# Optimization experiments

Measured on AMD Instinct MI355X. Metric: run time of the kernel, lower is better.

## Reference

```python
import jax, jax.numpy as jnp
import numpy as np

HID = 1024     # hidden_dim
HEADS = 8      # num_heads
HD = HID // HEADS  # head_dim = 128
MD = 8         # manifold_dim
L = 3          # num_layers
B, S = 8, 1024
EPS = 1e-7
BALL_MAX = 1.0 - 1e-5  # clamp inside Poincare ball (|curvature| = 1)


def expmap0(v):
    """Hyperbolic exponential map at origin, curvature -1 (Poincare ball)."""
    n = jnp.sqrt(jnp.sum(v * v, axis=-1, keepdims=True))
    n = jnp.maximum(n, EPS)
    return jnp.tanh(n) * v / n


def logmap0(y):
    """Hyperbolic logarithm map at origin, curvature -1 (Poincare ball)."""
    n = jnp.sqrt(jnp.sum(y * y, axis=-1, keepdims=True))
    n_c = jnp.clip(n, EPS, BALL_MAX)
    return jnp.arctanh(n_c) * y / n_c


def setup_inputs() -> dict:
    key = jax.random.key(0)
    ks = jax.random.split(key, 6)
    sc = 0.02
    return {
        "x": jax.random.normal(ks[0], (B, S, HID), dtype=jnp.float32),
        "W_qkv": jax.random.normal(ks[1], (HID, 3 * HID), dtype=jnp.float32) * sc,
        "b_qkv": jnp.zeros((3 * HID,), dtype=jnp.float32),
        "W_pinv": jax.random.normal(ks[2], (HID, MD), dtype=jnp.float32) * sc,
        "b_pinv": jnp.zeros((MD,), dtype=jnp.float32),
        "W_attn": jax.random.normal(ks[3], (L, MD, HID), dtype=jnp.float32) * sc,
        "b_attn": jnp.zeros((L, HID), dtype=jnp.float32),
        "W_out": jax.random.normal(ks[4], (HID, HID), dtype=jnp.float32) * sc,
        "b_out": jnp.zeros((HID,), dtype=jnp.float32),
    }


def reference(x, W_qkv, b_qkv, W_pinv, b_pinv, W_attn, b_attn, W_out, b_out):
    inv_sqrt_d = 1.0 / np.sqrt(HD).astype(np.float32)
    cur = x
    for l in range(L):
        qkv = jnp.einsum('bsh,hd->bsd', cur, W_qkv) + b_qkv  # [B,S,3*HID]
        q, k, v = jnp.split(qkv, 3, axis=-1)
        # [B,S,HID] -> [B,HEADS,S,HD]
        def heads(t):
            return t.reshape(B, S, HEADS, HD).transpose(0, 2, 1, 3)
        q, k, v = heads(q), heads(k), heads(v)
        # geometric 'flow': hyperbolic retraction of Q/K onto the Poincare ball
        # (parallel transport at the origin is identity)
        qf = expmap0(q)
        kf = expmap0(k)
        scores = jnp.einsum('bhqd,bhkd->bhqk', qf, kf) * inv_sqrt_d
        att = jax.nn.softmax(scores, axis=-1)
        o = jnp.einsum('bhqk,bhkd->bhqd', att, v)  # [B,H,S,HD]
        o = o.transpose(0, 2, 1, 3).reshape(B, S, HID)
        # project to manifold coords, then per-layer pattern projection back
        m = jnp.einsum('bsh,hm->bsm', o, W_pinv) + b_pinv           # [B,S,MD]
        upd = jnp.einsum('bsm,mh->bsh', m, W_attn[l]) + b_attn[l]   # [B,S,HID]
        cur = cur + upd
    return jnp.einsum('bsh,hd->bsd', cur, W_out) + b_out
```

## Files before the change

### kernel.cpp

```cpp
#include <hip/hip_runtime.h>
#include <hip/hip_bf16.h>
#include <hip/hip_fp8.h>
#include <cstdint>

typedef __hip_bfloat16 bf16;
typedef __bf16 b8 __attribute__((ext_vector_type(8)));
typedef float f4v __attribute__((ext_vector_type(4)));
typedef short s8v __attribute__((ext_vector_type(8)));
typedef int i8v __attribute__((ext_vector_type(8)));

#define DEVI static __device__ __forceinline__

DEVI void gload16(const void* g, void* l) {
  __builtin_amdgcn_global_load_lds(
      (const __attribute__((address_space(1))) void*)(uintptr_t)g,
      (__attribute__((address_space(3))) void*)(uint32_t)(uintptr_t)l,
      16, 0, 0);
}

DEVI f4v mfma_bf16(b8 a, b8 b, f4v c) {
  return __builtin_amdgcn_mfma_f32_16x16x32_bf16(a, b, c, 0, 0, 0);
}

DEVI f4v mfma_fp8(i8v a, i8v b, f4v c) {
  return __builtin_amdgcn_mfma_scale_f32_16x16x128_f8f6f4(
      a, b, c, 0, 0, 0, 0x7F7F7F7F, 0, 0x7F7F7F7F);
}

DEVI uint8_t to_fp8(float f) {
  __hip_fp8_e4m3 v(f);
  return v.__x;
}

__global__ void prep_kernel(const float* __restrict__ x, float* __restrict__ cur,
                            bf16* __restrict__ curb, uint8_t* __restrict__ curf8) {
  int i = (blockIdx.x * 256 + threadIdx.x) * 4;
  float4 v = *(const float4*)(x + i);
  *(float4*)(cur + i) = v;
  __hip_bfloat162 a, b;
  a.x = __float2bfloat16(v.x); a.y = __float2bfloat16(v.y);
  b.x = __float2bfloat16(v.z); b.y = __float2bfloat16(v.w);
  *(__hip_bfloat162*)(curb + i) = a;
  *(__hip_bfloat162*)(curb + i + 2) = b;
  uint32_t p = (uint32_t)to_fp8(v.x) | ((uint32_t)to_fp8(v.y) << 8) |
               ((uint32_t)to_fp8(v.z) << 16) | ((uint32_t)to_fp8(v.w) << 24);
  *(uint32_t*)(curf8 + i) = p;
}

__global__ void transpose_cast(const float* __restrict__ in, bf16* __restrict__ out,
                               int R, int C) {
  __shared__ float tile[32][33];
  int c0 = blockIdx.x * 32, r0 = blockIdx.y * 32;
  int tx = threadIdx.x & 31, ty = threadIdx.x >> 5;
  for (int rr = ty; rr < 32; rr += 8)
    tile[rr][tx] = in[(size_t)(r0 + rr) * C + c0 + tx];
  __syncthreads();
  for (int cc = ty; cc < 32; cc += 8)
    out[(size_t)(c0 + cc) * R + r0 + tx] = __float2bfloat16(tile[tx][cc]);
}

__global__ void transpose_cast_fp8(const float* __restrict__ in,
                                   uint8_t* __restrict__ out, int R, int C) {
  __shared__ float tile[32][33];
  int c0 = blockIdx.x * 32, r0 = blockIdx.y * 32;
  int tx = threadIdx.x & 31, ty = threadIdx.x >> 5;
  for (int rr = ty; rr < 32; rr += 8)
    tile[rr][tx] = in[(size_t)(r0 + rr) * C + c0 + tx];
  __syncthreads();
  for (int cc = ty; cc < 32; cc += 8)
    out[(size_t)(c0 + cc) * R + r0 + tx] = to_fp8(tile[tx][cc]);
}

__global__ __launch_bounds__(256, 3)
void gemm_qkv_fp8(const uint8_t* __restrict__ A, const uint8_t* __restrict__ Bt,
                  const float* __restrict__ bias, bf16* __restrict__ Qo,
                  bf16* __restrict__ Ko, bf16* __restrict__ Vto, int M, int N,
                  int K) {
  __shared__ uint8_t As[128 * 128];
  __shared__ uint8_t Bs[128 * 128];
  __shared__ float red[2][128];
  const int t = threadIdx.x;
  const int w = t >> 6, lane = t & 63;
  const int lm = lane & 15, qd = lane >> 4;
  const int m0 = blockIdx.x * 128, n0 = blockIdx.y * 128;
  const int wm = (w & 1) * 64, wn = (w >> 1) * 64;

  const uint8_t* Ag = A + (size_t)m0 * K;
  const uint8_t* Bg = Bt + (size_t)n0 * K;

  f4v acc[4][4];
  f4v zero = {0.f, 0.f, 0.f, 0.f};
#pragma unroll
  for (int i = 0; i < 4; i++)
#pragma unroll
    for (int j = 0; j < 4; j++) acc[i][j] = zero;

  for (int k0 = 0; k0 < K; k0 += 128) {
#pragma unroll
    for (int c = 0; c < 4; c++) {
      int s = c * 256 + t;
      int r = s >> 3;
      int kc = (s & 7) ^ (r & 7);
      gload16(Ag + (size_t)r * K + k0 + kc * 16, &As[s * 16]);
      gload16(Bg + (size_t)r * K + k0 + kc * 16, &Bs[s * 16]);
    }
    __syncthreads();
    i8v af[4], bfr[4];
#pragma unroll
    for (int tm = 0; tm < 4; tm++) {
      int row = wm + tm * 16 + lm;
      int ch = (qd * 2) ^ (row & 7);
      union { int4 q[2]; i8v v; } u;
      u.q[0] = *(const int4*)&As[row * 128 + ch * 16];
      u.q[1] = *(const int4*)&As[row * 128 + (ch ^ 1) * 16];
      af[tm] = u.v;
    }
#pragma unroll
    for (int tn = 0; tn < 4; tn++) {
      int row = wn + tn * 16 + lm;
      int ch = (qd * 2) ^ (row & 7);
      union { int4 q[2]; i8v v; } u;
      u.q[0] = *(const int4*)&Bs[row * 128 + ch * 16];
      u.q[1] = *(const int4*)&Bs[row * 128 + (ch ^ 1) * 16];
      bfr[tn] = u.v;
    }
#pragma unroll
    for (int tm = 0; tm < 4; tm++)
#pragma unroll
      for (int tn = 0; tn < 4; tn++)
        acc[tm][tn] = mfma_fp8(af[tm], bfr[tn], acc[tm][tn]);
    __syncthreads();
  }

  const int part = n0 >> 10;
  const int hh = (n0 >> 7) & 7;
  if (part == 2) {
#pragma unroll
    for (int tm = 0; tm < 4; tm++)
#pragma unroll
      for (int tn = 0; tn < 4; tn++) {
        int d = wn + tn * 16 + lm;
        float bv = bias[n0 + d];
        int row0 = m0 + wm + tm * 16 + qd * 4;
        int b = row0 >> 10, s0 = row0 & 1023;
        bf16 vt[4];
#pragma unroll
        for (int r = 0; r < 4; r++) vt[r] = __float2bfloat16(acc[tm][tn][r] + bv);
        *(ushort4*)&Vto[((size_t)(b * 8 + hh)) * 131072 + (size_t)d * 1024 + s0] =
            *(ushort4*)vt;
      }
  } else {
    float bvs[4];
#pragma unroll
    for (int tn = 0; tn < 4; tn++) bvs[tn] = bias[n0 + wn + tn * 16 + lm];
    float ss[4][4];
#pragma unroll
    for (int tm = 0; tm < 4; tm++)
#pragma unroll
      for (int r = 0; r < 4; r++) {
        float s = 0.f;
#pragma unroll
        for (int tn = 0; tn < 4; tn++) {
          float v = acc[tm][tn][r] + bvs[tn];
          s += v * v;
        }
#pragma unroll
        for (int off = 1; off < 16; off <<= 1) s += __shfl_xor(s, off, 64);
        ss[tm][r] = s;
      }
    if (lm == 0) {
#pragma unroll
      for (int tm = 0; tm < 4; tm++)
#pragma unroll
        for (int r = 0; r < 4; r++)
          red[w >> 1][wm + tm * 16 + qd * 4 + r] = ss[tm][r];
    }
    __syncthreads();
    const float qsc = (part == 0) ? 0.08838834764831845f : 1.0f;
    float scr[4][4];
#pragma unroll
    for (int tm = 0; tm < 4; tm++)
#pragma unroll
      for (int r = 0; r < 4; r++) {
        int row = wm + tm * 16 + qd * 4 + r;
        float tot = red[0][row] + red[1][row];
        float nrm = fmaxf(sqrtf(tot), 1e-7f);
        scr[tm][r] = tanhf(nrm) / nrm * qsc;
      }
    bf16* dst = (part == 0) ? Qo : Ko;
#pragma unroll
    for (int tm = 0; tm < 4; tm++)
#pragma unroll
      for (int tn = 0; tn < 4; tn++) {
        int d = wn + tn * 16 + lm;
        int row0 = m0 + wm + tm * 16 + qd * 4;
        int b = row0 >> 10, s0 = row0 & 1023;
#pragma unroll
        for (int r = 0; r < 4; r++)
          dst[(((size_t)(b * 8 + hh)) * 1024 + s0 + r) * 128 + d] =
              __float2bfloat16((acc[tm][tn][r] + bvs[tn]) * scr[tm][r]);
      }
  }
}

__global__ __launch_bounds__(256, 3)
void gemm_bt(const bf16* __restrict__ A, const bf16* __restrict__ Bt,
             const float* __restrict__ bias, float* __restrict__ Cf, int M, int N,
             int K) {
  __shared__ bf16 As[128 * 64];
  __shared__ bf16 Bs[128 * 64];
  const int t = threadIdx.x;
  const int w = t >> 6, lane = t & 63;
  const int lm = lane & 15, qd = lane >> 4;
  const int m0 = blockIdx.x * 128, n0 = blockIdx.y * 128;
  const int wm = (w & 1) * 64, wn = (w >> 1) * 64;

  const bf16* Ag = A + (size_t)m0 * K;
  const bf16* Bg = Bt + (size_t)n0 * K;

  f4v acc[4][4];
  f4v zero = {0.f, 0.f, 0.f, 0.f};
#pragma unroll
  for (int i = 0; i < 4; i++)
#pragma unroll
    for (int j = 0; j < 4; j++) acc[i][j] = zero;

  for (int k0 = 0; k0 < K; k0 += 64) {
#pragma unroll
    for (int c = 0; c < 4; c++) {
      int s = c * 256 + t;
      int r = s >> 3;
      int kc = (s & 7) ^ (r & 7);
      gload16(Ag + (size_t)r * K + k0 + kc * 8, &As[s * 8]);
      gload16(Bg + (size_t)r * K + k0 + kc * 8, &Bs[s * 8]);
    }
    __syncthreads();
#pragma unroll
    for (int ks = 0; ks < 2; ks++) {
      b8 af[4], bfr[4];
#pragma unroll
      for (int tm = 0; tm < 4; tm++) {
        int row = wm + tm * 16 + lm;
        int ch = (ks * 4 + qd) ^ (row & 7);
        af[tm] = *(const b8*)&As[row * 64 + ch * 8];
      }
#pragma unroll
      for (int tn = 0; tn < 4; tn++) {
        int row = wn + tn * 16 + lm;
        int ch = (ks * 4 + qd) ^ (row & 7);
        bfr[tn] = *(const b8*)&Bs[row * 64 + ch * 8];
      }
#pragma unroll
      for (int tm = 0; tm < 4; tm++)
#pragma unroll
        for (int tn = 0; tn < 4; tn++)
          acc[tm][tn] = mfma_bf16(af[tm], bfr[tn], acc[tm][tn]);
    }
    __syncthreads();
  }

#pragma unroll
  for (int tm = 0; tm < 4; tm++)
#pragma unroll
    for (int tn = 0; tn < 4; tn++) {
      int col = n0 + wn + tn * 16 + lm;
      float bv = bias[col];
#pragma unroll
      for (int r = 0; r < 4; r++) {
        int row = m0 + wm + tm * 16 + qd * 4 + r;
        Cf[(size_t)row * N + col] = acc[tm][tn][r] + bv;
      }
    }
}

__global__ __launch_bounds__(256, 2)
void attn_kernel(const bf16* __restrict__ Qf, const bf16* __restrict__ Kf,
                 const bf16* __restrict__ Vt, bf16* __restrict__ O) {
  __shared__ bf16 smem[40960];
  bf16* Ps = smem + 32768;
  const int t = threadIdx.x, w = t >> 6, lane = t & 63;
  const int lm = lane & 15, qd = lane >> 4;
  const int bh = blockIdx.x, qt = blockIdx.y;
  const bf16* Qg = Qf + ((size_t)bh * 1024 + qt * 128) * 128;
  const bf16* Kg = Kf + (size_t)bh * 131072;
  const bf16* Vg = Vt + (size_t)bh * 131072;
  bf16* Pw = Ps + w * 2048;

  auto stage = [&](int kt, int b) {
    bf16* Ksb = smem + b * 16384;
    bf16* Vsb = Ksb + 8192;
#pragma unroll
    for (int c = 0; c < 4; c++) {
      int s = c * 256 + t;
      int r = s >> 4;
      int kc = (s & 15) ^ (r & 7);
      gload16(Kg + (size_t)(kt * 64 + r) * 128 + kc * 8, &Ksb[s * 8]);
      int rv = s >> 3;
      int kv = (s & 7) ^ (rv & 7);
      gload16(Vg + (size_t)rv * 1024 + kt * 64 + kv * 8, &Vsb[s * 8]);
    }
  };

  b8 qfr[2][4];
#pragma unroll
  for (int mt = 0; mt < 2; mt++)
#pragma unroll
    for (int ks = 0; ks < 4; ks++)
      qfr[mt][ks] =
          *(const b8*)(Qg + (size_t)(w * 32 + mt * 16 + lm) * 128 + ks * 32 + qd * 8);

  f4v o[2][8];
  f4v lacc[2];
  f4v zero = {0.f, 0.f, 0.f, 0.f};
#pragma unroll
  for (int mt = 0; mt < 2; mt++) {
    lacc[mt] = zero;
#pragma unroll
    for (int i = 0; i < 8; i++) o[mt][i] = zero;
  }
  union { s8v s; b8 b; } uo;
#pragma unroll
  for (int i = 0; i < 8; i++) uo.s[i] = 0x3F80;
  const b8 ones = uo.b;

  stage(0, 0);
  for (int kt = 0; kt < 16; kt++) {
    const int cb = kt & 1;
    if (kt < 15) {
      stage(kt + 1, cb ^ 1);
      asm volatile("s_waitcnt vmcnt(8)" ::: "memory");
    } else {
      asm volatile("s_waitcnt vmcnt(0)" ::: "memory");
    }
    __builtin_amdgcn_sched_barrier(0);
    __builtin_amdgcn_s_barrier();
    __builtin_amdgcn_sched_barrier(0);
    const bf16* Ks = smem + cb * 16384;
    const bf16* Vs = Ks + 8192;

    f4v sc[2][4];
#pragma unroll
    for (int mt = 0; mt < 2; mt++)
#pragma unroll
      for (int tn = 0; tn < 4; tn++) sc[mt][tn] = zero;
#pragma unroll
    for (int tn = 0; tn < 4; tn++) {
      int krow = tn * 16 + lm;
#pragma unroll
      for (int ks = 0; ks < 4; ks++) {
        int ch = (ks * 4 + qd) ^ (krow & 7);
        b8 kfr = *(const b8*)&Ks[krow * 128 + ch * 8];
        sc[0][tn] = mfma_bf16(qfr[0][ks], kfr, sc[0][tn]);
        sc[1][tn] = mfma_bf16(qfr[1][ks], kfr, sc[1][tn]);
      }
    }
#pragma unroll
    for (int mt = 0; mt < 2; mt++)
#pragma unroll
      for (int tn = 0; tn < 4; tn++)
#pragma unroll
        for (int r = 0; r < 4; r++) {
          int qi = mt * 16 + qd * 4 + r;
          int ch = (tn * 2 + (lm >> 3)) ^ ((qi >> 1) & 7);
          Pw[qi * 64 + ch * 8 + (lm & 7)] = __float2bfloat16(__expf(sc[mt][tn][r]));
        }

    b8 pa[2][2];
#pragma unroll
    for (int mt = 0; mt < 2; mt++)
#pragma unroll
      for (int kv2 = 0; kv2 < 2; kv2++) {
        int qi = mt * 16 + lm;
        int ch = (kv2 * 4 + qd) ^ ((lm >> 1) & 7);
        pa[mt][kv2] = *(const b8*)&Pw[qi * 64 + ch * 8];
      }
#pragma unroll
    for (int mt = 0; mt < 2; mt++)
#pragma unroll
      for (int kv2 = 0; kv2 < 2; kv2++)
        lacc[mt] = mfma_bf16(pa[mt][kv2], ones, lacc[mt]);
#pragma unroll
    for (int tnd = 0; tnd < 8; tnd++) {
      int drow = tnd * 16 + lm;
#pragma unroll
      for (int kv2 = 0; kv2 < 2; kv2++) {
        int ch = (kv2 * 4 + qd) ^ (drow & 7);
        b8 vfr = *(const b8*)&Vs[drow * 64 + ch * 8];
#pragma unroll
        for (int mt = 0; mt < 2; mt++)
          o[mt][tnd] = mfma_bf16(pa[mt][kv2], vfr, o[mt][tnd]);
      }
    }
    __builtin_amdgcn_sched_barrier(0);
    __builtin_amdgcn_s_barrier();
  }

  const int b = bh >> 3, h = bh & 7;
#pragma unroll
  for (int mt = 0; mt < 2; mt++) {
    float rinv[4];
#pragma unroll
    for (int r = 0; r < 4; r++) rinv[r] = 1.0f / lacc[mt][r];
#pragma unroll
    for (int tnd = 0; tnd < 8; tnd++) {
      int d = tnd * 16 + lm;
#pragma unroll
      for (int r = 0; r < 4; r++) {
        int sIdx = qt * 128 + w * 32 + mt * 16 + qd * 4 + r;
        O[((size_t)b * 1024 + sIdx) * 1024 + h * 128 + d] =
            __float2bfloat16(o[mt][tnd][r] * rinv[r]);
      }
    }
  }
}

__global__ __launch_bounds__(256)
void update_kernel(const bf16* __restrict__ O, const float* __restrict__ Wpinv,
                   const float* __restrict__ bpinv, const float* __restrict__ Wattn,
                   const float* __restrict__ battn, float* __restrict__ cur,
                   bf16* __restrict__ curb, uint8_t* __restrict__ curf8) {
  const int row = blockIdx.x;
  const int t = threadIdx.x, w = t >> 6, lane = t & 63;
  const int h0 = t * 4;
  const bf16* orow = O + (size_t)row * 1024;

  bf16 ob[4];
  *(ushort4*)ob = *(const ushort4*)(orow + h0);
  float ov[4];
#pragma unroll
  for (int i = 0; i < 4; i++) ov[i] = __bfloat162float(ob[i]);

  float acc[8];
#pragma unroll
  for (int j = 0; j < 8; j++) acc[j] = 0.f;
#pragma unroll
  for (int i = 0; i < 4; i++) {
    float4 wa = *(const float4*)(Wpinv + (size_t)(h0 + i) * 8);
    float4 wb = *(const float4*)(Wpinv + (size_t)(h0 + i) * 8 + 4);
    acc[0] += ov[i] * wa.x; acc[1] += ov[i] * wa.y;
    acc[2] += ov[i] * wa.z; acc[3] += ov[i] * wa.w;
    acc[4] += ov[i] * wb.x; acc[5] += ov[i] * wb.y;
    acc[6] += ov[i] * wb.z; acc[7] += ov[i] * wb.w;
  }
#pragma unroll
  for (int j = 0; j < 8; j++)
#pragma unroll
    for (int off = 32; off; off >>= 1) acc[j] += __shfl_xor(acc[j], off, 64);
  __shared__ float sm[4][8];
  if (lane == 0) {
#pragma unroll
    for (int j = 0; j < 8; j++) sm[w][j] = acc[j];
  }
  __syncthreads();
  float mv[8];
#pragma unroll
  for (int j = 0; j < 8; j++)
    mv[j] = sm[0][j] + sm[1][j] + sm[2][j] + sm[3][j] + bpinv[j];

  float u[4];
#pragma unroll
  for (int i = 0; i < 4; i++) u[i] = battn[h0 + i];
#pragma unroll
  for (int j = 0; j < 8; j++) {
    float4 wv = *(const float4*)(Wattn + (size_t)j * 1024 + h0);
    u[0] += mv[j] * wv.x; u[1] += mv[j] * wv.y;
    u[2] += mv[j] * wv.z; u[3] += mv[j] * wv.w;
  }
  float4 c4 = *(float4*)(cur + (size_t)row * 1024 + h0);
  c4.x += u[0]; c4.y += u[1]; c4.z += u[2]; c4.w += u[3];
  *(float4*)(cur + (size_t)row * 1024 + h0) = c4;
  bf16 cb[4];
  cb[0] = __float2bfloat16(c4.x); cb[1] = __float2bfloat16(c4.y);
  cb[2] = __float2bfloat16(c4.z); cb[3] = __float2bfloat16(c4.w);
  *(ushort4*)(curb + (size_t)row * 1024 + h0) = *(ushort4*)cb;
  uint32_t p = (uint32_t)to_fp8(c4.x) | ((uint32_t)to_fp8(c4.y) << 8) |
               ((uint32_t)to_fp8(c4.z) << 16) | ((uint32_t)to_fp8(c4.w) << 24);
  *(uint32_t*)(curf8 + (size_t)row * 1024 + h0) = p;
}

extern "C" void kernel_launch(void* const* d_in, const int* in_sizes, int n_in,
                              void* d_out, int out_size, void* d_ws, size_t ws_size,
                              hipStream_t stream) {
  const float* x      = (const float*)d_in[0];
  const float* W_qkv  = (const float*)d_in[1];
  const float* b_qkv  = (const float*)d_in[2];
  const float* W_pinv = (const float*)d_in[3];
  const float* b_pinv = (const float*)d_in[4];
  const float* W_attn = (const float*)d_in[5];
  const float* b_attn = (const float*)d_in[6];
  const float* W_out  = (const float*)d_in[7];
  const float* b_out  = (const float*)d_in[8];

  char* ws = (char*)d_ws;
  size_t off = 0;
  auto alloc = [&](size_t bytes) -> void* {
    void* p = ws + off;
    off += (bytes + 255) & ~(size_t)255;
    return p;
  };
  float* cur     = (float*)alloc((size_t)8192 * 1024 * 4);
  bf16* curb     = (bf16*)alloc((size_t)8192 * 1024 * 2);
  uint8_t* curf8 = (uint8_t*)alloc((size_t)8192 * 1024);
  uint8_t* Wqkv8 = (uint8_t*)alloc((size_t)3072 * 1024);
  bf16* Woutt    = (bf16*)alloc((size_t)1024 * 1024 * 2);
  bf16* Q        = (bf16*)alloc((size_t)8192 * 1024 * 2);
  bf16* Kt       = (bf16*)alloc((size_t)8192 * 1024 * 2);
  bf16* Vt       = (bf16*)alloc((size_t)8192 * 1024 * 2);
  bf16* O        = (bf16*)alloc((size_t)8192 * 1024 * 2);
  (void)ws_size; (void)in_sizes; (void)n_in; (void)out_size;

  prep_kernel<<<8192, 256, 0, stream>>>(x, cur, curb, curf8);
  transpose_cast_fp8<<<dim3(96, 32), 256, 0, stream>>>(W_qkv, Wqkv8, 1024, 3072);
  transpose_cast<<<dim3(32, 32), 256, 0, stream>>>(W_out, Woutt, 1024, 1024);

  for (int l = 0; l < 3; l++) {
    gemm_qkv_fp8<<<dim3(64, 24), 256, 0, stream>>>(curf8, Wqkv8, b_qkv, Q, Kt, Vt,
                                                   8192, 3072, 1024);
    attn_kernel<<<dim3(64, 8), 256, 0, stream>>>(Q, Kt, Vt, O);
    update_kernel<<<8192, 256, 0, stream>>>(O, W_pinv, b_pinv,
                                            W_attn + (size_t)l * 8 * 1024,
                                            b_attn + (size_t)l * 1024, cur, curb,
                                            curf8);
  }
  gemm_bt<<<dim3(64, 8), 256, 0, stream>>>(curb, Woutt, b_out, (float*)d_out, 8192,
                                           1024, 1024);
}
```

Baseline: 523.6 us.

## Split attention query tile across 8 waves of 16 rows each

```diff
diff --git a/kernel.cpp b/kernel.cpp
--- a/kernel.cpp
+++ b/kernel.cpp
@@ -273,7 +273,7 @@
     }
 }
 
-__global__ __launch_bounds__(256, 2)
+__global__ __launch_bounds__(512, 4)
 void attn_kernel(const bf16* __restrict__ Qf, const bf16* __restrict__ Kf,
                  const bf16* __restrict__ Vt, bf16* __restrict__ O) {
   __shared__ bf16 smem[40960];
@@ -284,14 +284,14 @@
   const bf16* Qg = Qf + ((size_t)bh * 1024 + qt * 128) * 128;
   const bf16* Kg = Kf + (size_t)bh * 131072;
   const bf16* Vg = Vt + (size_t)bh * 131072;
-  bf16* Pw = Ps + w * 2048;
+  bf16* Pw = Ps + w * 1024;
 
   auto stage = [&](int kt, int b) {
     bf16* Ksb = smem + b * 16384;
     bf16* Vsb = Ksb + 8192;
 #pragma unroll
-    for (int c = 0; c < 4; c++) {
-      int s = c * 256 + t;
+    for (int c = 0; c < 2; c++) {
+      int s = c * 512 + t;
       int r = s >> 4;
       int kc = (s & 15) ^ (r & 7);
       gload16(Kg + (size_t)(kt * 64 + r) * 128 + kc * 8, &Ksb[s * 8]);
@@ -301,23 +301,17 @@
     }
   };
 
-  b8 qfr[2][4];
-#pragma unroll
-  for (int mt = 0; mt < 2; mt++)
-#pragma unroll
-    for (int ks = 0; ks < 4; ks++)
-      qfr[mt][ks] =
-          *(const b8*)(Qg + (size_t)(w * 32 + mt * 16 + lm) * 128 + ks * 32 + qd * 8);
-
-  f4v o[2][8];
-  f4v lacc[2];
+  b8 qfr[4];
+#pragma unroll
+  for (int ks = 0; ks < 4; ks++)
+    qfr[ks] = *(const b8*)(Qg + (size_t)(w * 16 + lm) * 128 + ks * 32 + qd * 8);
+
+  f4v o[8];
+  f4v lacc;
   f4v zero = {0.f, 0.f, 0.f, 0.f};
-#pragma unroll
-  for (int mt = 0; mt < 2; mt++) {
-    lacc[mt] = zero;
-#pragma unroll
-    for (int i = 0; i < 8; i++) o[mt][i] = zero;
-  }
+  lacc = zero;
+#pragma unroll
+  for (int i = 0; i < 8; i++) o[i] = zero;
   union { s8v s; b8 b; } uo;
 #pragma unroll
   for (int i = 0; i < 8; i++) uo.s[i] = 0x3F80;
@@ -328,7 +322,7 @@
     const int cb = kt & 1;
     if (kt < 15) {
       stage(kt + 1, cb ^ 1);
-      asm volatile("s_waitcnt vmcnt(8)" ::: "memory");
+      asm volatile("s_waitcnt vmcnt(4)" ::: "memory");
     } else {
       asm volatile("s_waitcnt vmcnt(0)" ::: "memory");
     }
@@ -338,11 +332,9 @@
     const bf16* Ks = smem + cb * 16384;
     const bf16* Vs = Ks + 8192;
 
-    f4v sc[2][4];
-#pragma unroll
-    for (int mt = 0; mt < 2; mt++)
-#pragma unroll
-      for (int tn = 0; tn < 4; tn++) sc[mt][tn] = zero;
+    f4v sc[4];
+#pragma unroll
+    for (int tn = 0; tn < 4; tn++) sc[tn] = zero;
 #pragma unroll
     for (int tn = 0; tn < 4; tn++) {
       int krow = tn * 16 + lm;
@@ -350,35 +342,27 @@
       for (int ks = 0; ks < 4; ks++) {
         int ch = (ks * 4 + qd) ^ (krow & 7);
         b8 kfr = *(const b8*)&Ks[krow * 128 + ch * 8];
-        sc[0][tn] = mfma_bf16(qfr[0][ks], kfr, sc[0][tn]);
-        sc[1][tn] = mfma_bf16(qfr[1][ks], kfr, sc[1][tn]);
-      }
-    }
-#pragma unroll
-    for (int mt = 0; mt < 2; mt++)
-#pragma unroll
-      for (int tn = 0; tn < 4; tn++)
-#pragma unroll
-        for (int r = 0; r < 4; r++) {
-          int qi = mt * 16 + qd * 4 + r;
-          int ch = (tn * 2 + (lm >> 3)) ^ ((qi >> 1) & 7);
-          Pw[qi * 64 + ch * 8 + (lm & 7)] = __float2bfloat16(__expf(sc[mt][tn][r]));
-        }
-
-    b8 pa[2][2];
-#pragma unroll
-    for (int mt = 0; mt < 2; mt++)
-#pragma unroll
-      for (int kv2 = 0; kv2 < 2; kv2++) {
-        int qi = mt * 16 + lm;
-        int ch = (kv2 * 4 + qd) ^ ((lm >> 1) & 7);
-        pa[mt][kv2] = *(const b8*)&Pw[qi * 64 + ch * 8];
-      }
-#pragma unroll
-    for (int mt = 0; mt < 2; mt++)
-#pragma unroll
-      for (int kv2 = 0; kv2 < 2; kv2++)
-        lacc[mt] = mfma_bf16(pa[mt][kv2], ones, lacc[mt]);
+        sc[tn] = mfma_bf16(qfr[ks], kfr, sc[tn]);
+      }
+    }
+#pragma unroll
+    for (int tn = 0; tn < 4; tn++)
+#pragma unroll
+      for (int r = 0; r < 4; r++) {
+        int qi = qd * 4 + r;
+        int ch = (tn * 2 + (lm >> 3)) ^ ((qi >> 1) & 7);
+        Pw[qi * 64 + ch * 8 + (lm & 7)] = __float2bfloat16(__expf(sc[tn][r]));
+      }
+
+    b8 pa[2];
+#pragma unroll
+    for (int kv2 = 0; kv2 < 2; kv2++) {
+      int qi = lm;
+      int ch = (kv2 * 4 + qd) ^ ((lm >> 1) & 7);
+      pa[kv2] = *(const b8*)&Pw[qi * 64 + ch * 8];
+    }
+#pragma unroll
+    for (int kv2 = 0; kv2 < 2; kv2++) lacc = mfma_bf16(pa[kv2], ones, lacc);
 #pragma unroll
     for (int tnd = 0; tnd < 8; tnd++) {
       int drow = tnd * 16 + lm;
@@ -386,9 +370,7 @@
       for (int kv2 = 0; kv2 < 2; kv2++) {
         int ch = (kv2 * 4 + qd) ^ (drow & 7);
         b8 vfr = *(const b8*)&Vs[drow * 64 + ch * 8];
-#pragma unroll
-        for (int mt = 0; mt < 2; mt++)
-          o[mt][tnd] = mfma_bf16(pa[mt][kv2], vfr, o[mt][tnd]);
+        o[tnd] = mfma_bf16(pa[kv2], vfr, o[tnd]);
       }
     }
     __builtin_amdgcn_sched_barrier(0);
@@ -396,20 +378,17 @@
   }
 
   const int b = bh >> 3, h = bh & 7;
-#pragma unroll
-  for (int mt = 0; mt < 2; mt++) {
-    float rinv[4];
-#pragma unroll
-    for (int r = 0; r < 4; r++) rinv[r] = 1.0f / lacc[mt][r];
-#pragma unroll
-    for (int tnd = 0; tnd < 8; tnd++) {
-      int d = tnd * 16 + lm;
-#pragma unroll
-      for (int r = 0; r < 4; r++) {
-        int sIdx = qt * 128 + w * 32 + mt * 16 + qd * 4 + r;
-        O[((size_t)b * 1024 + sIdx) * 1024 + h * 128 + d] =
-            __float2bfloat16(o[mt][tnd][r] * rinv[r]);
-      }
+  float rinv[4];
+#pragma unroll
+  for (int r = 0; r < 4; r++) rinv[r] = 1.0f / lacc[r];
+#pragma unroll
+  for (int tnd = 0; tnd < 8; tnd++) {
+    int d = tnd * 16 + lm;
+#pragma unroll
+    for (int r = 0; r < 4; r++) {
+      int sIdx = qt * 128 + w * 16 + qd * 4 + r;
+      O[((size_t)b * 1024 + sIdx) * 1024 + h * 128 + d] =
+          __float2bfloat16(o[tnd][r] * rinv[r]);
     }
   }
 }
@@ -516,7 +495,7 @@
   for (int l = 0; l < 3; l++) {
     gemm_qkv_fp8<<<dim3(64, 24), 256, 0, stream>>>(curf8, Wqkv8, b_qkv, Q, Kt, Vt,
                                                    8192, 3072, 1024);
-    attn_kernel<<<dim3(64, 8), 256, 0, stream>>>(Q, Kt, Vt, O);
+    attn_kernel<<<dim3(64, 8), 512, 0, stream>>>(Q, Kt, Vt, O);
     update_kernel<<<8192, 256, 0, stream>>>(O, W_pinv, b_pinv,
                                             W_attn + (size_t)l * 8 * 1024,
                                             b_attn + (size_t)l * 1024, cur, curb,
```

Result: no change. 523.9 us (+0.1%).

## Double-buffer LDS tiles in FP8 QKV GEMM to overlap loads with MFMA

Applied to the files above, without the earlier changes.

```diff
diff --git a/kernel.cpp b/kernel.cpp
--- a/kernel.cpp
+++ b/kernel.cpp
@@ -71,13 +71,13 @@
     out[(size_t)(c0 + cc) * R + r0 + tx] = to_fp8(tile[tx][cc]);
 }
 
-__global__ __launch_bounds__(256, 3)
+__global__ __launch_bounds__(256, 2)
 void gemm_qkv_fp8(const uint8_t* __restrict__ A, const uint8_t* __restrict__ Bt,
                   const float* __restrict__ bias, bf16* __restrict__ Qo,
                   bf16* __restrict__ Ko, bf16* __restrict__ Vto, int M, int N,
                   int K) {
-  __shared__ uint8_t As[128 * 128];
-  __shared__ uint8_t Bs[128 * 128];
+  __shared__ uint8_t As[2][128 * 128];
+  __shared__ uint8_t Bs[2][128 * 128];
   __shared__ float red[2][128];
   const int t = threadIdx.x;
   const int w = t >> 6, lane = t & 63;
@@ -88,31 +88,46 @@
   const uint8_t* Ag = A + (size_t)m0 * K;
   const uint8_t* Bg = Bt + (size_t)n0 * K;
 
-  f4v acc[4][4];
-  f4v zero = {0.f, 0.f, 0.f, 0.f};
-#pragma unroll
-  for (int i = 0; i < 4; i++)
-#pragma unroll
-    for (int j = 0; j < 4; j++) acc[i][j] = zero;
-
-  for (int k0 = 0; k0 < K; k0 += 128) {
+  auto stage = [&](int k0, int b) {
 #pragma unroll
     for (int c = 0; c < 4; c++) {
       int s = c * 256 + t;
       int r = s >> 3;
       int kc = (s & 7) ^ (r & 7);
-      gload16(Ag + (size_t)r * K + k0 + kc * 16, &As[s * 16]);
-      gload16(Bg + (size_t)r * K + k0 + kc * 16, &Bs[s * 16]);
-    }
-    __syncthreads();
+      gload16(Ag + (size_t)r * K + k0 + kc * 16, &As[b][s * 16]);
+      gload16(Bg + (size_t)r * K + k0 + kc * 16, &Bs[b][s * 16]);
+    }
+  };
+
+  f4v acc[4][4];
+  f4v zero = {0.f, 0.f, 0.f, 0.f};
+#pragma unroll
+  for (int i = 0; i < 4; i++)
+#pragma unroll
+    for (int j = 0; j < 4; j++) acc[i][j] = zero;
+
+  const int NT = K >> 7;
+  stage(0, 0);
+  for (int it = 0; it < NT; it++) {
+    const int cb = it & 1;
+    if (it < NT - 1) {
+      stage((it + 1) << 7, cb ^ 1);
+      asm volatile("s_waitcnt vmcnt(8)" ::: "memory");
+    } else {
+      asm volatile("s_waitcnt vmcnt(0)" ::: "memory");
+    }
+    __builtin_amdgcn_sched_barrier(0);
+    __builtin_amdgcn_s_barrier();
+    __builtin_amdgcn_sched_barrier(0);
+
     i8v af[4], bfr[4];
 #pragma unroll
     for (int tm = 0; tm < 4; tm++) {
       int row = wm + tm * 16 + lm;
       int ch = (qd * 2) ^ (row & 7);
       union { int4 q[2]; i8v v; } u;
-      u.q[0] = *(const int4*)&As[row * 128 + ch * 16];
-      u.q[1] = *(const int4*)&As[row * 128 + (ch ^ 1) * 16];
+      u.q[0] = *(const int4*)&As[cb][row * 128 + ch * 16];
+      u.q[1] = *(const int4*)&As[cb][row * 128 + (ch ^ 1) * 16];
       af[tm] = u.v;
     }
 #pragma unroll
@@ -120,8 +135,8 @@
       int row = wn + tn * 16 + lm;
       int ch = (qd * 2) ^ (row & 7);
       union { int4 q[2]; i8v v; } u;
-      u.q[0] = *(const int4*)&Bs[row * 128 + ch * 16];
-      u.q[1] = *(const int4*)&Bs[row * 128 + (ch ^ 1) * 16];
+      u.q[0] = *(const int4*)&Bs[cb][row * 128 + ch * 16];
+      u.q[1] = *(const int4*)&Bs[cb][row * 128 + (ch ^ 1) * 16];
       bfr[tn] = u.v;
     }
 #pragma unroll
@@ -129,7 +144,9 @@
 #pragma unroll
       for (int tn = 0; tn < 4; tn++)
         acc[tm][tn] = mfma_fp8(af[tm], bfr[tn], acc[tm][tn]);
-    __syncthreads();
+
+    __builtin_amdgcn_sched_barrier(0);
+    __builtin_amdgcn_s_barrier();
   }
 
   const int part = n0 >> 10;
```

New measurement: 564.8 us. +7.9%, slower.
